# Kernel optimization log

Hardware: AMD Instinct MI355X
Metric: run time of the kernel (lower is better)

The kernel has to match this reference:

```python
import jax, jax.numpy as jnp
import numpy as np

N_NODES = 50000
N_EDGES = 600000
D_IN = 128
D_OUT = 128
EPS = 1e-5


def setup_inputs() -> dict:
    key = jax.random.key(0)
    k1, k2, k3 = jax.random.split(key, 3)
    x = jax.random.normal(k1, (N_NODES, D_IN), dtype=jnp.float32)
    # GCNConv linear weight (bias=False), applied as x @ W.T
    W = jax.random.normal(k2, (D_OUT, D_IN), dtype=jnp.float32) * (1.0 / np.sqrt(D_IN))
    edge_index = jax.random.randint(k3, (2, N_EDGES), 0, N_NODES, dtype=jnp.int64)
    return {"x": x, "W": W, "edge_index": edge_index}


def reference(x, W, edge_index):
    N = x.shape[0]
    dtype = x.dtype
    # --- GCNConv: add self loops, symmetric normalization, gather-scatter ---
    loop = jnp.arange(N, dtype=edge_index.dtype)
    row = jnp.concatenate([edge_index[0], loop])  # source nodes
    col = jnp.concatenate([edge_index[1], loop])  # target nodes (aggregation)
    ew = jnp.ones(row.shape[0], dtype=dtype)
    deg = jax.ops.segment_sum(ew, col, num_segments=N)  # in-degree incl. self loops
    dinv = jnp.where(deg > 0, jax.lax.rsqrt(deg), 0.0)
    norm = dinv[row] * dinv[col]  # [E+N]
    xw = x @ W.T  # [N, D_OUT]
    msg = xw[row] * norm[:, None]  # gather + edge scaling
    out = jax.ops.segment_sum(msg, col, num_segments=N)  # scatter-add aggregation
    # --- PairNorm (scale=1.0, scale_individually=False) ---
    xc = out - out.mean(axis=0, keepdims=True)
    out = xc / jnp.sqrt(EPS + jnp.mean(jnp.sum(xc * xc, axis=-1)))
    # --- activation + residual ---
    return jax.nn.relu(out) + out
```

## Files before the change

### kernel.cpp

```cpp
#include <hip/hip_runtime.h>
#include <hip/hip_fp16.h>

#define EPS 1e-5f
#define NREP 16
#define REPSTRIDE 132
#define MAXDEG 48

typedef _Float16 half8_t __attribute__((ext_vector_type(8)));
typedef float floatx4 __attribute__((ext_vector_type(4)));

__global__ void scatter_kernel(const int* __restrict__ row, const int* __restrict__ col,
                               int* __restrict__ cursor, int* __restrict__ csr, int E) {
    int e = blockIdx.x * blockDim.x + threadIdx.x;
    if (e < E) {
        int c = col[e];
        int pos = atomicAdd(&cursor[c], 1);
        if (pos < MAXDEG) csr[c * MAXDEG + pos] = row[e];
    }
}

__global__ __launch_bounds__(256) void gemm_kernel(
    const float* __restrict__ x, const float* __restrict__ W,
    const int* __restrict__ cursor, __half* __restrict__ xsh, int N) {
    __shared__ _Float16 sw[128][136];

    int tid = threadIdx.x;
#pragma unroll
    for (int t = 0; t < 16; ++t) {
        int idx = tid + t * 256;
        int j = idx >> 5;
        int k4 = idx & 31;
        float4 v = ((const float4*)W)[idx];
        _Float16* d = &sw[j][k4 * 4];
        d[0] = (_Float16)v.x; d[1] = (_Float16)v.y;
        d[2] = (_Float16)v.z; d[3] = (_Float16)v.w;
    }
    __syncthreads();

    int w  = tid >> 6;
    int l  = tid & 63;
    int lr = l & 15;
    int kb = l >> 4;

    int rowA = blockIdx.x * 64 + w * 16 + lr;
    const float4* xr = (const float4*)&x[(size_t)min(rowA, N - 1) * 128];

    float4 xv[8];
#pragma unroll
    for (int kk = 0; kk < 4; ++kk) {
        xv[2 * kk]     = xr[8 * kk + 2 * kb];
        xv[2 * kk + 1] = xr[8 * kk + 2 * kb + 1];
    }
    half8_t a[4];
#pragma unroll
    for (int kk = 0; kk < 4; ++kk) {
        float4 v0 = xv[2 * kk], v1 = xv[2 * kk + 1];
        half8_t h;
        h[0] = (_Float16)v0.x; h[1] = (_Float16)v0.y;
        h[2] = (_Float16)v0.z; h[3] = (_Float16)v0.w;
        h[4] = (_Float16)v1.x; h[5] = (_Float16)v1.y;
        h[6] = (_Float16)v1.z; h[7] = (_Float16)v1.w;
        a[kk] = h;
    }

    floatx4 acc[8];
#pragma unroll
    for (int t = 0; t < 8; ++t) acc[t] = (floatx4){0.f, 0.f, 0.f, 0.f};

#pragma unroll
    for (int kk = 0; kk < 4; ++kk) {
#pragma unroll
        for (int t = 0; t < 8; ++t) {
            half8_t b = *(const half8_t*)&sw[16 * t + lr][32 * kk + 8 * kb];
            acc[t] = __builtin_amdgcn_mfma_f32_16x16x32_f16(a[kk], b, acc[t], 0, 0, 0);
        }
    }

    int rbase = blockIdx.x * 64 + w * 16 + 4 * kb;
    float dv[4];
#pragma unroll
    for (int r = 0; r < 4; ++r)
        dv[r] = (rbase + r < N) ? rsqrtf((float)(cursor[rbase + r] + 1)) : 0.f;
#pragma unroll
    for (int r = 0; r < 4; ++r) {
        int grow = rbase + r;
        if (grow < N) {
#pragma unroll
            for (int t = 0; t < 8; ++t)
                xsh[(size_t)grow * 128 + 16 * t + lr] = __float2half(acc[t][r] * dv[r]);
        }
    }
}

__global__ void gather_kernel(const __half2* __restrict__ xs2, const int* __restrict__ cursor,
                              const int* __restrict__ csr,
                              float* __restrict__ pre, float* __restrict__ colrep,
                              float* __restrict__ ssrep, int N) {
    __shared__ float scol[128];
    __shared__ float sss;
    if (threadIdx.x < 128) scol[threadIdx.x] = 0.f;
    if (threadIdx.x == 0) sss = 0.f;
    __syncthreads();

    int lane = threadIdx.x & 63;
    int wid = (blockIdx.x * blockDim.x + threadIdx.x) >> 6;
    int nw  = (gridDim.x * blockDim.x) >> 6;
    float2* pre2 = (float2*)pre;
    float csx = 0.f, csy = 0.f, ss = 0.f;

    for (int n = wid; n < N; n += nw) {
        int deg = cursor[n];
        int e = min(deg, MAXDEG);
        const int* cs = &csr[n * MAXDEG];
        float2 acc = __half22float2(xs2[n * 64 + lane]);
        for (int base = 0; base < e; base += 16) {
            int idx[16];
#pragma unroll
            for (int t = 0; t < 16; ++t) idx[t] = cs[min(base + t, e - 1)];
            __half2 a[16];
#pragma unroll
            for (int t = 0; t < 16; ++t) a[t] = xs2[idx[t] * 64 + lane];
#pragma unroll
            for (int t = 0; t < 16; ++t) {
                float m = (base + t < e) ? 1.f : 0.f;
                float2 f = __half22float2(a[t]);
                acc.x += m * f.x; acc.y += m * f.y;
            }
        }
        float dv = rsqrtf((float)(deg + 1));
        float vx = acc.x * dv, vy = acc.y * dv;
        pre2[n * 64 + lane] = make_float2(vx, vy);
        csx += vx; csy += vy; ss += vx * vx + vy * vy;
    }

    atomicAdd(&scol[2 * lane], csx);
    atomicAdd(&scol[2 * lane + 1], csy);
    for (int d = 32; d > 0; d >>= 1) ss += __shfl_down(ss, d);
    if (lane == 0) atomicAdd(&sss, ss);
    __syncthreads();
    int rep = blockIdx.x & (NREP - 1);
    if (threadIdx.x < 128) atomicAdd(&colrep[rep * REPSTRIDE + threadIdx.x], scol[threadIdx.x]);
    if (threadIdx.x == 128) atomicAdd(&ssrep[rep], sss);
}

__global__ void final_kernel(float* __restrict__ out, const float* __restrict__ colrep,
                             const float* __restrict__ ssrep, int N, int total) {
    __shared__ float sm[128];
    __shared__ float red[128];
    __shared__ float sscale;
    int t = threadIdx.x;
    if (t < 128) {
        float cs = 0.f;
#pragma unroll
        for (int r = 0; r < NREP; ++r) cs += colrep[r * REPSTRIDE + t];
        float m = cs / (float)N;
        sm[t] = m;
        red[t] = m * m;
    }
    __syncthreads();
    for (int d = 64; d > 0; d >>= 1) {
        if (t < d) red[t] += red[t + d];
        __syncthreads();
    }
    if (t == 0) {
        float sq = 0.f;
#pragma unroll
        for (int r = 0; r < NREP; ++r) sq += ssrep[r];
        float tot = sq - (float)N * red[0];
        sscale = rsqrtf(EPS + tot / (float)N);
    }
    __syncthreads();
    float s = sscale;
    int tid = blockIdx.x * blockDim.x + threadIdx.x;
    int stride = gridDim.x * blockDim.x;
    for (int i = tid; i < total; i += stride) {
        float y = (out[i] - sm[i & 127]) * s;
        out[i] = y > 0.f ? 2.f * y : y;
    }
}

extern "C" void kernel_launch(void* const* d_in, const int* in_sizes, int n_in,
                              void* d_out, int out_size, void* d_ws, size_t ws_size,
                              hipStream_t stream) {
    const float* x = (const float*)d_in[0];
    const float* W = (const float*)d_in[1];
    const int* ei  = (const int*)d_in[2];
    int N = in_sizes[0] / 128;
    int E = in_sizes[2] / 2;
    const int* row = ei;
    const int* col = ei + E;
    float* out = (float*)d_out;

    __half* xsh      = (__half*)d_ws;
    int*   cursor    = (int*)((float*)d_ws + (size_t)N * 64);
    float* colrep    = (float*)(cursor + N);
    float* ssrep     = colrep + NREP * REPSTRIDE;
    int*   csr       = (int*)(ssrep + NREP);

    hipMemsetAsync(cursor, 0, (size_t)(N + NREP * REPSTRIDE + NREP) * 4, stream);

    scatter_kernel<<<(E + 255) / 256, 256, 0, stream>>>(row, col, cursor, csr, E);
    gemm_kernel   <<<(N + 63) / 64, 256, 0, stream>>>(x, W, cursor, xsh, N);
    gather_kernel <<<2048, 256, 0, stream>>>((const __half2*)xsh, cursor, csr,
                                             out, colrep, ssrep, N);
    final_kernel  <<<1024, 256, 0, stream>>>(out, colrep, ssrep, N, N * 128);
}
```

Before: 177.8 us.

## Fuse CSR scatter and GEMM into one interleaved launch, move source norm to gather

The edge-scatter (CSR build) and the x@W^T GEMM now run as one kernel, with three of every four blocks doing scatter and the fourth doing GEMM, so the two independent phases overlap. The GEMM no longer depends on degrees, so the source-side rsqrt(deg) scaling moves into the gather loop, which now reads cursor[idx] for every neighbour. This removes one launch and the serialization between the two phases. In exchange the gather does an extra random 4-byte load and an rsqrt per edge, and the GEMM output is stored unscaled in fp16.

```diff
diff --git a/kernel.cpp b/kernel.cpp
--- a/kernel.cpp
+++ b/kernel.cpp
@@ -9,22 +9,31 @@
 typedef _Float16 half8_t __attribute__((ext_vector_type(8)));
 typedef float floatx4 __attribute__((ext_vector_type(4)));
 
-__global__ void scatter_kernel(const int* __restrict__ row, const int* __restrict__ col,
-                               int* __restrict__ cursor, int* __restrict__ csr, int E) {
-    int e = blockIdx.x * blockDim.x + threadIdx.x;
-    if (e < E) {
-        int c = col[e];
-        int pos = atomicAdd(&cursor[c], 1);
-        if (pos < MAXDEG) csr[c * MAXDEG + pos] = row[e];
-    }
-}
-
-__global__ __launch_bounds__(256) void gemm_kernel(
+__global__ __launch_bounds__(256) void build_kernel(
+    const int* __restrict__ row, const int* __restrict__ col,
+    int* __restrict__ cursor, int* __restrict__ csr, int E, int nScatter,
     const float* __restrict__ x, const float* __restrict__ W,
-    const int* __restrict__ cursor, __half* __restrict__ xsh, int N) {
+    __half* __restrict__ xsh, int N, int nGemm) {
     __shared__ _Float16 sw[128][136];
 
+    int b = blockIdx.x;
     int tid = threadIdx.x;
+
+    if ((b & 3) != 3) {
+        int sb = b - ((b + 1) >> 2);
+        if (sb >= nScatter) return;
+        int e = sb * 256 + tid;
+        if (e < E) {
+            int c = col[e];
+            int pos = atomicAdd(&cursor[c], 1);
+            if (pos < MAXDEG) csr[c * MAXDEG + pos] = row[e];
+        }
+        return;
+    }
+
+    int gb = b >> 2;
+    if (gb >= nGemm) return;
+
 #pragma unroll
     for (int t = 0; t < 16; ++t) {
         int idx = tid + t * 256;
@@ -42,7 +51,7 @@
     int lr = l & 15;
     int kb = l >> 4;
 
-    int rowA = blockIdx.x * 64 + w * 16 + lr;
+    int rowA = gb * 64 + w * 16 + lr;
     const float4* xr = (const float4*)&x[(size_t)min(rowA, N - 1) * 128];
 
     float4 xv[8];
@@ -71,23 +80,19 @@
     for (int kk = 0; kk < 4; ++kk) {
 #pragma unroll
         for (int t = 0; t < 8; ++t) {
-            half8_t b = *(const half8_t*)&sw[16 * t + lr][32 * kk + 8 * kb];
-            acc[t] = __builtin_amdgcn_mfma_f32_16x16x32_f16(a[kk], b, acc[t], 0, 0, 0);
-        }
-    }
-
-    int rbase = blockIdx.x * 64 + w * 16 + 4 * kb;
-    float dv[4];
-#pragma unroll
-    for (int r = 0; r < 4; ++r)
-        dv[r] = (rbase + r < N) ? rsqrtf((float)(cursor[rbase + r] + 1)) : 0.f;
+            half8_t bb = *(const half8_t*)&sw[16 * t + lr][32 * kk + 8 * kb];
+            acc[t] = __builtin_amdgcn_mfma_f32_16x16x32_f16(a[kk], bb, acc[t], 0, 0, 0);
+        }
+    }
+
+    int rbase = gb * 64 + w * 16 + 4 * kb;
 #pragma unroll
     for (int r = 0; r < 4; ++r) {
         int grow = rbase + r;
         if (grow < N) {
 #pragma unroll
             for (int t = 0; t < 8; ++t)
-                xsh[(size_t)grow * 128 + 16 * t + lr] = __float2half(acc[t][r] * dv[r]);
+                xsh[(size_t)grow * 128 + 16 * t + lr] = __float2half(acc[t][r]);
         }
     }
 }
@@ -112,7 +117,9 @@
         int deg = cursor[n];
         int e = min(deg, MAXDEG);
         const int* cs = &csr[n * MAXDEG];
-        float2 acc = __half22float2(xs2[n * 64 + lane]);
+        float dvn = rsqrtf((float)(deg + 1));
+        float2 sf = __half22float2(xs2[n * 64 + lane]);
+        float accx = sf.x * dvn, accy = sf.y * dvn;
         for (int base = 0; base < e; base += 16) {
             int idx[16];
 #pragma unroll
@@ -120,15 +127,19 @@
             __half2 a[16];
 #pragma unroll
             for (int t = 0; t < 16; ++t) a[t] = xs2[idx[t] * 64 + lane];
+            float dvt[16];
 #pragma unroll
             for (int t = 0; t < 16; ++t) {
-                float m = (base + t < e) ? 1.f : 0.f;
+                int dg = cursor[idx[t]];
+                dvt[t] = (base + t < e) ? rsqrtf((float)(dg + 1)) : 0.f;
+            }
+#pragma unroll
+            for (int t = 0; t < 16; ++t) {
                 float2 f = __half22float2(a[t]);
-                acc.x += m * f.x; acc.y += m * f.y;
+                accx += dvt[t] * f.x; accy += dvt[t] * f.y;
             }
         }
-        float dv = rsqrtf((float)(deg + 1));
-        float vx = acc.x * dv, vy = acc.y * dv;
+        float vx = accx * dvn, vy = accy * dvn;
         pre2[n * 64 + lane] = make_float2(vx, vy);
         csx += vx; csy += vy; ss += vx * vx + vy * vy;
     }
@@ -199,8 +210,13 @@
 
     hipMemsetAsync(cursor, 0, (size_t)(N + NREP * REPSTRIDE + NREP) * 4, stream);
 
-    scatter_kernel<<<(E + 255) / 256, 256, 0, stream>>>(row, col, cursor, csr, E);
-    gemm_kernel   <<<(N + 63) / 64, 256, 0, stream>>>(x, W, cursor, xsh, N);
+    int nScatter = (E + 255) / 256;
+    int nGemm    = (N + 63) / 64;
+    int nsBlk    = (nScatter + 2) / 3;
+    int tot      = 4 * (nGemm > nsBlk ? nGemm : nsBlk);
+
+    build_kernel  <<<tot, 256, 0, stream>>>(row, col, cursor, csr, E, nScatter,
+                                            x, W, xsh, N, nGemm);
     gather_kernel <<<2048, 256, 0, stream>>>((const __half2*)xsh, cursor, csr,
                                              out, colrep, ssrep, N);
     final_kernel  <<<1024, 256, 0, stream>>>(out, colrep, ssrep, N, N * 128);
```

New measurement: 221.6 us. 24.7% more time.

## Software-pipeline gather loop: prefetch next node's indices and neighbor rows

Applied to the files above, without the earlier changes.

Restructures the per-node gather loop into a two-stage software pipeline. The CSR indices, degree and self row are prefetched two nodes ahead, and the first 16 neighbor feature rows one node ahead. This hides the dependent index-then-data load latency behind the current node's accumulation. It costs extra registers (two 16-entry arrays per lane), which may reduce occupancy, and it reads csr slots past the degree even though those reads are masked.

```diff
diff --git a/kernel.cpp b/kernel.cpp
--- a/kernel.cpp
+++ b/kernel.cpp
@@ -108,25 +108,81 @@
     float2* pre2 = (float2*)pre;
     float csx = 0.f, csy = 0.f, ss = 0.f;
 
+    int iDeg = 0; __half2 iSelf = __half2{}; int iIdx[16];
+    int vDeg = 0; __half2 vSelf = __half2{}; __half2 vVals[16];
+#pragma unroll
+    for (int t = 0; t < 16; ++t) iIdx[t] = 0;
+#pragma unroll
+    for (int t = 0; t < 16; ++t) vVals[t] = __half2{};
+
+    if (wid < N) {
+        iDeg = cursor[wid];
+        iSelf = xs2[wid * 64 + lane];
+        const int* cs0 = &csr[wid * MAXDEG];
+#pragma unroll
+        for (int t = 0; t < 16; ++t) iIdx[t] = cs0[t];
+        int e0 = min(iDeg, MAXDEG);
+        int safe = (e0 > 0) ? iIdx[0] : wid;
+        vDeg = iDeg; vSelf = iSelf;
+#pragma unroll
+        for (int t = 0; t < 16; ++t)
+            vVals[t] = xs2[((t < e0) ? iIdx[t] : safe) * 64 + lane];
+        int n1 = wid + nw;
+        if (n1 < N) {
+            iDeg = cursor[n1];
+            iSelf = xs2[n1 * 64 + lane];
+            const int* cs1 = &csr[n1 * MAXDEG];
+#pragma unroll
+            for (int t = 0; t < 16; ++t) iIdx[t] = cs1[t];
+        }
+    }
+
     for (int n = wid; n < N; n += nw) {
-        int deg = cursor[n];
+        int deg = vDeg;
         int e = min(deg, MAXDEG);
-        const int* cs = &csr[n * MAXDEG];
-        float2 acc = __half22float2(xs2[n * 64 + lane]);
-        for (int base = 0; base < e; base += 16) {
-            int idx[16];
-#pragma unroll
-            for (int t = 0; t < 16; ++t) idx[t] = cs[min(base + t, e - 1)];
-            __half2 a[16];
-#pragma unroll
-            for (int t = 0; t < 16; ++t) a[t] = xs2[idx[t] * 64 + lane];
-#pragma unroll
-            for (int t = 0; t < 16; ++t) {
-                float m = (base + t < e) ? 1.f : 0.f;
-                float2 f = __half22float2(a[t]);
-                acc.x += m * f.x; acc.y += m * f.y;
+        float2 acc = __half22float2(vSelf);
+#pragma unroll
+        for (int t = 0; t < 16; ++t) {
+            float m = (t < e) ? 1.f : 0.f;
+            float2 f = __half22float2(vVals[t]);
+            acc.x += m * f.x; acc.y += m * f.y;
+        }
+        if (e > 16) {
+            const int* cs = &csr[n * MAXDEG];
+            for (int base = 16; base < e; base += 16) {
+                int idx[16];
+#pragma unroll
+                for (int t = 0; t < 16; ++t) idx[t] = cs[min(base + t, e - 1)];
+                __half2 b[16];
+#pragma unroll
+                for (int t = 0; t < 16; ++t) b[t] = xs2[idx[t] * 64 + lane];
+#pragma unroll
+                for (int t = 0; t < 16; ++t) {
+                    float m = (base + t < e) ? 1.f : 0.f;
+                    float2 f = __half22float2(b[t]);
+                    acc.x += m * f.x; acc.y += m * f.y;
+                }
             }
         }
+
+        int nn = n + nw;
+        if (nn < N) {
+            int e1 = min(iDeg, MAXDEG);
+            int safe = (e1 > 0) ? iIdx[0] : nn;
+            vDeg = iDeg; vSelf = iSelf;
+#pragma unroll
+            for (int t = 0; t < 16; ++t)
+                vVals[t] = xs2[((t < e1) ? iIdx[t] : safe) * 64 + lane];
+        }
+        int n2 = n + 2 * nw;
+        if (n2 < N) {
+            iDeg = cursor[n2];
+            iSelf = xs2[n2 * 64 + lane];
+            const int* cs2 = &csr[n2 * MAXDEG];
+#pragma unroll
+            for (int t = 0; t < 16; ++t) iIdx[t] = cs2[t];
+        }
+
         float dv = rsqrtf((float)(deg + 1));
         float vx = acc.x * dv, vy = acc.y * dv;
         pre2[n * 64 + lane] = make_float2(vx, vy);
```

Result: faster. 172.2 us (-3.1%).
